# Performance work log

Hardware: AMD Instinct MI355X
Metric: run time of the kernel (lower is better)

Reference implementation:

```python
import jax, jax.numpy as jnp
import numpy as np

# Block-sparse layout constants (must match init_kwargs):
BS = 64       # block_size (= block_m = block_n)
NB = 64       # number of blocks per side -> max_seqlen = 4096
LOCAL = 8     # causal sliding window of 8 blocks
GLOBAL = 1    # 1 global (attention-sink) block


def _layout():
    """Build padded per-row block column indices and the token-level mask.

    Mirrors dkernel semantics: block (i, j) participates iff sparse_pattern[i, j] == 1,
    and within participating blocks a per-token causal mask (k_pos <= q_pos) is applied
    (dkernel applies causal masking on diagonal blocks; off-diagonal lower blocks pass
    the causal test trivially, so pattern & causal is exact).
    """
    i = np.arange(NB)[:, None]
    j = np.arange(NB)[None, :]
    pat = (j <= i) & (((i - j) < LOCAL) | (j < GLOBAL))  # [NB, NB] bool
    max_nnz = int(pat.sum(-1).max())                      # = LOCAL + GLOBAL = 9
    col = np.zeros((NB, max_nnz), np.int32)
    valid = np.zeros((NB, max_nnz), bool)
    for r in range(NB):
        idx = np.nonzero(pat[r])[0]
        col[r, :len(idx)] = idx
        valid[r, :len(idx)] = True
    # token positions
    qpos = np.arange(NB)[:, None] * BS + np.arange(BS)[None, :]                    # [NB, BS]
    kpos = (col[:, :, None] * BS + np.arange(BS)[None, None, :]).reshape(NB, -1)   # [NB, max_nnz*BS]
    vmask = np.repeat(valid, BS, axis=1)                                           # [NB, max_nnz*BS]
    mask = vmask[:, None, :] & (kpos[:, None, :] <= qpos[:, :, None])              # [NB, BS, max_nnz*BS]
    return col, mask

_COL, _MASK = _layout()


def setup_inputs() -> dict:
    key = jax.random.key(0)
    kq, kk, kv = jax.random.split(key, 3)
    B, S, H, D = 2, 4096, 16, 128
    q = jax.random.normal(kq, (B, S, H, D), dtype=jnp.float32)
    k = jax.random.normal(kk, (B, S, H, D), dtype=jnp.float32)
    v = jax.random.normal(kv, (B, S, H, D), dtype=jnp.float32)
    return {"q": q, "k": k, "v": v}


def reference(q, k, v):
    B, S, H, D = q.shape
    sm_scale = 1.0 / np.sqrt(float(D))  # default sm_scale in forward()
    # -> [B, H, NB, BS, D]
    qb = q.reshape(B, NB, BS, H, D).transpose(0, 3, 1, 2, 4)
    kb = k.reshape(B, NB, BS, H, D).transpose(0, 3, 1, 2, 4)
    vb = v.reshape(B, NB, BS, H, D).transpose(0, 3, 1, 2, 4)
    col = jnp.asarray(_COL)                              # [NB, max_nnz]
    # gather the kv blocks each q-block attends to: [B, H, NB, max_nnz*BS, D]
    kg = kb[:, :, col].reshape(B, H, NB, -1, D)
    vg = vb[:, :, col].reshape(B, H, NB, -1, D)
    # block-sparse scores: [B, H, NB, BS, max_nnz*BS]
    s = jnp.einsum('bhnqd,bhnkd->bhnqk', qb, kg) * sm_scale
    s = jnp.where(jnp.asarray(_MASK)[None, None], s, -jnp.inf)
    p = jax.nn.softmax(s, axis=-1)
    o = jnp.einsum('bhnqk,bhnkd->bhnqd', p, vg)          # [B, H, NB, BS, D]
    return o.transpose(0, 2, 3, 1, 4).reshape(B, S, H, D)
```

## Files before the change

kernel.cpp:

```cpp
#include <hip/hip_runtime.h>
#include <hip/hip_bf16.h>


typedef __bf16 bf16_t;
typedef bf16_t bf16x8 __attribute__((ext_vector_type(8)));
typedef float f32x4 __attribute__((ext_vector_type(4)));
typedef uint32_t u32x4 __attribute__((ext_vector_type(4)));

#define BSZ 64
#define DIM 128
#define NH 16
#define SEQ 4096
#define ROWSTRIDE (NH * DIM)

#define LGKM_BARRIER()                                          \
    do {                                                        \
        asm volatile("s_waitcnt lgkmcnt(0)" ::: "memory");      \
        __builtin_amdgcn_s_barrier();                           \
    } while (0)

__device__ __forceinline__ uint32_t cvt_pk_bf16(float lo, float hi) {
    uint32_t r;
    asm("v_cvt_pk_bf16_f32 %0, %1, %2" : "=v"(r) : "v"(lo), "v"(hi));
    return r;
}

__device__ __forceinline__ uint32_t kb_swz(uint32_t A) {
    return A ^ (((A >> 8) & 7u) << 4) ^ (((A >> 11) & 1u) << 7);
}
__device__ __forceinline__ uint32_t vt_swz(uint32_t A) {
    return A ^ (((A >> 9) & 7u) << 4) ^ (((A >> 9) & 1u) << 6) ^ (((A >> 12) & 3u) << 7);
}

__global__ __launch_bounds__(256) void sparse_attn_kernel(
    const float* __restrict__ q, const float* __restrict__ k,
    const float* __restrict__ v, float* __restrict__ out)
{
    __shared__ __align__(16) bf16_t Kb[BSZ * DIM];
    __shared__ __align__(16) bf16_t Vt[DIM * BSZ];

    const int L  = ((blockIdx.x & 7) << 8) | (blockIdx.x >> 3);
    const int qi = L & 63;
    const int h  = (L >> 6) & 15;
    const int b  = L >> 10;

    const int tid  = threadIdx.x;
    const int wave = tid >> 6;
    const int lane = tid & 63;
    const int lr = lane & 15;
    const int lk = lane >> 4;
    const int k0 = lk * 8;

    const int krr = tid >> 4;
    const int kc8 = tid & 15;
    const int vr  = tid >> 5;
    const int sc4 = tid & 31;

    const float scale2 = 0.12751649736230476f;

    const size_t bh_off = ((size_t)b * SEQ * NH + (size_t)h) * DIM;
    const float* kbh = k + bh_off;
    const float* vbh = v + bh_off;

    bf16x8 qf[4];
    {
        const float* qrow = q + bh_off + (size_t)(qi * 64 + wave * 16 + lr) * ROWSTRIDE;
        #pragma unroll
        for (int kk = 0; kk < 4; ++kk) {
            const float4 a0 = *(const float4*)(qrow + 32 * kk + k0);
            const float4 a1 = *(const float4*)(qrow + 32 * kk + k0 + 4);
            u32x4 w = {cvt_pk_bf16(a0.x * scale2, a0.y * scale2),
                       cvt_pk_bf16(a0.z * scale2, a0.w * scale2),
                       cvt_pk_bf16(a1.x * scale2, a1.y * scale2),
                       cvt_pk_bf16(a1.z * scale2, a1.w * scale2)};
            qf[kk] = *(bf16x8*)&w;
        }
    }

    f32x4 oacc[8];
    #pragma unroll
    for (int n = 0; n < 8; ++n) oacc[n] = (f32x4){0.f, 0.f, 0.f, 0.f};
    float lrun = 0.f;

    const int qrow_local = wave * 16 + lr;
    const int nnz = (qi < 8) ? (qi + 1) : 9;

    const int bit0 = lk & 1;
    const int bit1 = lk >> 1;
    const bool hi  = (lk & 2) != 0;
    const int Dlo  = (lr + 16 * bit1) << 2;
    const int Dhi  = Dlo + (32 << 2);
    const int addrA = bit0 ? Dhi : Dlo;
    const int addrB = bit0 ? Dlo : Dhi;

    float4 kreg[8];
    float4 vreg[8];

    #define LOAD_K(jb)                                                            \
    {                                                                             \
        _Pragma("unroll")                                                         \
        for (int i = 0; i < 4; ++i) {                                             \
            const float* p_ = kbh + (size_t)((jb) * 64 + 16 * i + krr) * ROWSTRIDE\
                              + 8 * kc8;                                          \
            kreg[2 * i]     = *(const float4*)(p_);                               \
            kreg[2 * i + 1] = *(const float4*)(p_ + 4);                           \
        }                                                                         \
    }
    #define LOAD_V(jb)                                                            \
    {                                                                             \
        const float* vb_ = vbh + (size_t)((jb) * 64 + 8 * vr) * ROWSTRIDE + 4 * sc4;\
        _Pragma("unroll")                                                         \
        for (int i = 0; i < 8; ++i)                                               \
            vreg[i] = *(const float4*)(vb_ + (size_t)i * ROWSTRIDE);              \
    }

    LOAD_K(0);
    LOAD_V(0);

    for (int t = 0; t < nnz; ++t) {
        const int j = (qi < 8) ? t : ((t == 0) ? 0 : (qi - 8 + t));
        const int jn = (qi < 8) ? (t + 1) : (qi - 8 + t + 1);
        const bool have_next = (t + 1 < nnz);

        #pragma unroll
        for (int i = 0; i < 4; ++i) {
            const float4 a0 = kreg[2 * i];
            const float4 a1 = kreg[2 * i + 1];
            u32x4 w = {cvt_pk_bf16(a0.x, a0.y), cvt_pk_bf16(a0.z, a0.w),
                       cvt_pk_bf16(a1.x, a1.y), cvt_pk_bf16(a1.z, a1.w)};
            const uint32_t A = kb_swz((uint32_t)((16 * i + krr) * 256 + 16 * kc8));
            *(u32x4*)((char*)Kb + A) = w;
        }
        if (have_next) { LOAD_K(jn); }

        LGKM_BARRIER();

        f32x4 sacc[4];
        #pragma unroll
        for (int n = 0; n < 4; ++n) {
            f32x4 a = (f32x4){0.f, 0.f, 0.f, 0.f};
            #pragma unroll
            for (int kk = 0; kk < 4; ++kk) {
                const uint32_t A = kb_swz((uint32_t)((16 * n + lr) * 256 + 64 * kk + 16 * lk));
                bf16x8 kf = *(const bf16x8*)((const char*)Kb + A);
                a = __builtin_amdgcn_mfma_f32_16x16x32_bf16(kf, qf[kk], a, 0, 0, 0);
            }
            sacc[n] = a;
        }

        #pragma unroll
        for (int j2 = 0; j2 < 4; ++j2) {
            u32x4 w = {cvt_pk_bf16(((const float*)&vreg[0])[j2], ((const float*)&vreg[1])[j2]),
                       cvt_pk_bf16(((const float*)&vreg[2])[j2], ((const float*)&vreg[3])[j2]),
                       cvt_pk_bf16(((const float*)&vreg[4])[j2], ((const float*)&vreg[5])[j2]),
                       cvt_pk_bf16(((const float*)&vreg[6])[j2], ((const float*)&vreg[7])[j2])};
            const int d = 4 * sc4 + j2;
            const uint32_t A = vt_swz((uint32_t)(d * 128 + 16 * vr));
            *(u32x4*)((char*)Vt + A) = w;
        }
        if (have_next) { LOAD_V(jn); }

        if (j == qi) {
            #pragma unroll
            for (int n = 0; n < 4; ++n)
                #pragma unroll
                for (int r = 0; r < 4; ++r) {
                    if (16 * n + 4 * lk + r > qrow_local) sacc[n][r] = -1.0e30f;
                }
        }

        uint32_t ch[8];
        #pragma unroll
        for (int n = 0; n < 4; ++n) {
            float p0 = exp2f(sacc[n][0]);
            float p1 = exp2f(sacc[n][1]);
            float p2 = exp2f(sacc[n][2]);
            float p3 = exp2f(sacc[n][3]);
            lrun += (p0 + p1) + (p2 + p3);
            ch[2 * n]     = cvt_pk_bf16(p0, p1);
            ch[2 * n + 1] = cvt_pk_bf16(p2, p3);
        }

        bf16x8 paf[2];
        #pragma unroll
        for (int kk = 0; kk < 2; ++kk) {
            uint32_t r0 = (uint32_t)__builtin_amdgcn_ds_permute(
                addrA, (int)(bit0 ? ch[4 * kk + 2] : ch[4 * kk + 0]));
            uint32_t r1 = (uint32_t)__builtin_amdgcn_ds_permute(
                addrA, (int)(bit0 ? ch[4 * kk + 3] : ch[4 * kk + 1]));
            uint32_t r2 = (uint32_t)__builtin_amdgcn_ds_permute(
                addrB, (int)(bit0 ? ch[4 * kk + 0] : ch[4 * kk + 2]));
            uint32_t r3 = (uint32_t)__builtin_amdgcn_ds_permute(
                addrB, (int)(bit0 ? ch[4 * kk + 1] : ch[4 * kk + 3]));
            u32x4 tv = {hi ? r2 : r0, hi ? r3 : r1,
                        hi ? r0 : r2, hi ? r1 : r3};
            paf[kk] = *(bf16x8*)&tv;
        }

        LGKM_BARRIER();

        #pragma unroll
        for (int n = 0; n < 8; ++n) {
            f32x4 a = oacc[n];
            #pragma unroll
            for (int kk = 0; kk < 2; ++kk) {
                const uint32_t Av = vt_swz((uint32_t)((16 * n + lr) * 128 + 64 * kk + 16 * lk));
                bf16x8 vf = *(const bf16x8*)((const char*)Vt + Av);
                a = __builtin_amdgcn_mfma_f32_16x16x32_bf16(paf[kk], vf, a, 0, 0, 0);
            }
            oacc[n] = a;
        }
    }

    float lrtot = lrun;
    lrtot += __shfl_xor(lrtot, 16);
    lrtot += __shfl_xor(lrtot, 32);
    float* obase = out + bh_off + (size_t)(qi * 64 + wave * 16) * ROWSTRIDE;
    #pragma unroll
    for (int r = 0; r < 4; ++r) {
        const float inv = 1.0f / __shfl(lrtot, 4 * lk + r);
        float* orow = obase + (size_t)(4 * lk + r) * ROWSTRIDE;
        #pragma unroll
        for (int n = 0; n < 8; ++n) {
            orow[16 * n + lr] = oacc[n][r] * inv;
        }
    }
}

extern "C" void kernel_launch(void* const* d_in, const int* in_sizes, int n_in,
                              void* d_out, int out_size, void* d_ws, size_t ws_size,
                              hipStream_t stream) {
    const float* q = (const float*)d_in[0];
    const float* k = (const float*)d_in[1];
    const float* v = (const float*)d_in[2];
    float* out = (float*)d_out;
    sparse_attn_kernel<<<dim3(2048), dim3(256), 0, stream>>>(q, k, v, out);
}
```

Before: 92.53 us.

## Add dedicated producer wave group with double-buffered K/V shared memory

Splits the block into four consumer waves that do the MFMA work and two producer waves that load K/V from global memory, convert them to bf16 and write them into double-buffered shared memory. Consumers no longer hold prefetch registers or do conversions, and producers and consumers hand off each block through one barrier per iteration. The aim is to overlap global loads and conversion with compute while cutting consumer register pressure. In exchange, shared memory per block doubles to 64KB and the block grows to 384 threads, which may lower occupancy, and the producers load serially in large batches.

```diff
diff --git a/kernel.cpp b/kernel.cpp
--- a/kernel.cpp
+++ b/kernel.cpp
@@ -32,35 +32,100 @@
     return A ^ (((A >> 9) & 7u) << 4) ^ (((A >> 9) & 1u) << 6) ^ (((A >> 12) & 3u) << 7);
 }
 
-__global__ __launch_bounds__(256) void sparse_attn_kernel(
+__global__ __launch_bounds__(384) void sparse_attn_kernel(
     const float* __restrict__ q, const float* __restrict__ k,
     const float* __restrict__ v, float* __restrict__ out)
 {
-    __shared__ __align__(16) bf16_t Kb[BSZ * DIM];
-    __shared__ __align__(16) bf16_t Vt[DIM * BSZ];
+    __shared__ __align__(16) bf16_t Kb[2 * BSZ * DIM];
+    __shared__ __align__(16) bf16_t Vt[2 * DIM * BSZ];
 
     const int L  = ((blockIdx.x & 7) << 8) | (blockIdx.x >> 3);
     const int qi = L & 63;
     const int h  = (L >> 6) & 15;
     const int b  = L >> 10;
 
-    const int tid  = threadIdx.x;
+    const int tid = threadIdx.x;
+
+    const size_t bh_off = ((size_t)b * SEQ * NH + (size_t)h) * DIM;
+    const float* kbh = k + bh_off;
+    const float* vbh = v + bh_off;
+    const int nnz = (qi < 8) ? (qi + 1) : 9;
+
+    if (tid >= 256) {
+        const int pl   = tid - 256;
+        const int krow = pl >> 4;
+        const int kch8 = pl & 15;
+        const int vrb  = pl >> 5;
+        const int sc4p = pl & 31;
+
+        #define PROD_STAGE(jb, bufOff)                                            \
+        {                                                                         \
+            const float* kb_ = kbh + (size_t)(jb) * 64 * ROWSTRIDE;               \
+            const float* vb_ = vbh + (size_t)(jb) * 64 * ROWSTRIDE;               \
+            float4 st[16];                                                        \
+            _Pragma("unroll")                                                     \
+            for (int i = 0; i < 8; ++i) {                                         \
+                const float* p_ = kb_ + (size_t)(krow + 8 * i) * ROWSTRIDE        \
+                                  + 8 * kch8;                                     \
+                st[2 * i]     = *(const float4*)p_;                               \
+                st[2 * i + 1] = *(const float4*)(p_ + 4);                         \
+            }                                                                     \
+            _Pragma("unroll")                                                     \
+            for (int i = 0; i < 8; ++i) {                                         \
+                const float4 a0 = st[2 * i], a1 = st[2 * i + 1];                  \
+                u32x4 w = {cvt_pk_bf16(a0.x, a0.y), cvt_pk_bf16(a0.z, a0.w),      \
+                           cvt_pk_bf16(a1.x, a1.y), cvt_pk_bf16(a1.z, a1.w)};     \
+                const uint32_t A = kb_swz((uint32_t)((krow + 8 * i) * 256         \
+                                                     + 16 * kch8));               \
+                *(u32x4*)((char*)Kb + (bufOff) + A) = w;                          \
+            }                                                                     \
+            _Pragma("unroll")                                                     \
+            for (int g = 0; g < 2; ++g) {                                         \
+                const int vrg = vrb + 4 * g;                                      \
+                const float* q_ = vb_ + (size_t)(8 * vrg) * ROWSTRIDE + 4 * sc4p; \
+                _Pragma("unroll")                                                 \
+                for (int i = 0; i < 8; ++i)                                       \
+                    st[8 * g + i] = *(const float4*)(q_ + (size_t)i * ROWSTRIDE); \
+            }                                                                     \
+            _Pragma("unroll")                                                     \
+            for (int g = 0; g < 2; ++g) {                                         \
+                const int vrg = vrb + 4 * g;                                      \
+                _Pragma("unroll")                                                 \
+                for (int j2 = 0; j2 < 4; ++j2) {                                  \
+                    u32x4 w = {cvt_pk_bf16(((const float*)&st[8*g+0])[j2],        \
+                                           ((const float*)&st[8*g+1])[j2]),       \
+                               cvt_pk_bf16(((const float*)&st[8*g+2])[j2],        \
+                                           ((const float*)&st[8*g+3])[j2]),       \
+                               cvt_pk_bf16(((const float*)&st[8*g+4])[j2],        \
+                                           ((const float*)&st[8*g+5])[j2]),       \
+                               cvt_pk_bf16(((const float*)&st[8*g+6])[j2],        \
+                                           ((const float*)&st[8*g+7])[j2])};      \
+                    const int d = 4 * sc4p + j2;                                  \
+                    const uint32_t A = vt_swz((uint32_t)(d * 128 + 16 * vrg));    \
+                    *(u32x4*)((char*)Vt + (bufOff) + A) = w;                      \
+                }                                                                 \
+            }                                                                     \
+        }
+
+        PROD_STAGE(0, 0);
+        LGKM_BARRIER();
+        for (int t = 0; t < nnz; ++t) {
+            if (t + 1 < nnz) {
+                const int jn = (qi < 8) ? (t + 1) : (qi - 8 + t + 1);
+                PROD_STAGE(jn, (uint32_t)(((t + 1) & 1) * 16384));
+            }
+            LGKM_BARRIER();
+        }
+        return;
+    }
+
     const int wave = tid >> 6;
     const int lane = tid & 63;
     const int lr = lane & 15;
     const int lk = lane >> 4;
     const int k0 = lk * 8;
 
-    const int krr = tid >> 4;
-    const int kc8 = tid & 15;
-    const int vr  = tid >> 5;
-    const int sc4 = tid & 31;
-
     const float scale2 = 0.12751649736230476f;
-
-    const size_t bh_off = ((size_t)b * SEQ * NH + (size_t)h) * DIM;
-    const float* kbh = k + bh_off;
-    const float* vbh = v + bh_off;
 
     bf16x8 qf[4];
     {
@@ -83,7 +148,6 @@
     float lrun = 0.f;
 
     const int qrow_local = wave * 16 + lr;
-    const int nnz = (qi < 8) ? (qi + 1) : 9;
 
     const int bit0 = lk & 1;
     const int bit1 = lk >> 1;
@@ -93,47 +157,11 @@
     const int addrA = bit0 ? Dhi : Dlo;
     const int addrB = bit0 ? Dlo : Dhi;
 
-    float4 kreg[8];
-    float4 vreg[8];
-
-    #define LOAD_K(jb)                                                            \
-    {                                                                             \
-        _Pragma("unroll")                                                         \
-        for (int i = 0; i < 4; ++i) {                                             \
-            const float* p_ = kbh + (size_t)((jb) * 64 + 16 * i + krr) * ROWSTRIDE\
-                              + 8 * kc8;                                          \
-            kreg[2 * i]     = *(const float4*)(p_);                               \
-            kreg[2 * i + 1] = *(const float4*)(p_ + 4);                           \
-        }                                                                         \
-    }
-    #define LOAD_V(jb)                                                            \
-    {                                                                             \
-        const float* vb_ = vbh + (size_t)((jb) * 64 + 8 * vr) * ROWSTRIDE + 4 * sc4;\
-        _Pragma("unroll")                                                         \
-        for (int i = 0; i < 8; ++i)                                               \
-            vreg[i] = *(const float4*)(vb_ + (size_t)i * ROWSTRIDE);              \
-    }
-
-    LOAD_K(0);
-    LOAD_V(0);
+    LGKM_BARRIER();
 
     for (int t = 0; t < nnz; ++t) {
         const int j = (qi < 8) ? t : ((t == 0) ? 0 : (qi - 8 + t));
-        const int jn = (qi < 8) ? (t + 1) : (qi - 8 + t + 1);
-        const bool have_next = (t + 1 < nnz);
-
-        #pragma unroll
-        for (int i = 0; i < 4; ++i) {
-            const float4 a0 = kreg[2 * i];
-            const float4 a1 = kreg[2 * i + 1];
-            u32x4 w = {cvt_pk_bf16(a0.x, a0.y), cvt_pk_bf16(a0.z, a0.w),
-                       cvt_pk_bf16(a1.x, a1.y), cvt_pk_bf16(a1.z, a1.w)};
-            const uint32_t A = kb_swz((uint32_t)((16 * i + krr) * 256 + 16 * kc8));
-            *(u32x4*)((char*)Kb + A) = w;
-        }
-        if (have_next) { LOAD_K(jn); }
-
-        LGKM_BARRIER();
+        const uint32_t bufOff = (uint32_t)((t & 1) * 16384);
 
         f32x4 sacc[4];
         #pragma unroll
@@ -142,23 +170,11 @@
             #pragma unroll
             for (int kk = 0; kk < 4; ++kk) {
                 const uint32_t A = kb_swz((uint32_t)((16 * n + lr) * 256 + 64 * kk + 16 * lk));
-                bf16x8 kf = *(const bf16x8*)((const char*)Kb + A);
+                bf16x8 kf = *(const bf16x8*)((const char*)Kb + bufOff + A);
                 a = __builtin_amdgcn_mfma_f32_16x16x32_bf16(kf, qf[kk], a, 0, 0, 0);
             }
             sacc[n] = a;
         }
-
-        #pragma unroll
-        for (int j2 = 0; j2 < 4; ++j2) {
-            u32x4 w = {cvt_pk_bf16(((const float*)&vreg[0])[j2], ((const float*)&vreg[1])[j2]),
-                       cvt_pk_bf16(((const float*)&vreg[2])[j2], ((const float*)&vreg[3])[j2]),
-                       cvt_pk_bf16(((const float*)&vreg[4])[j2], ((const float*)&vreg[5])[j2]),
-                       cvt_pk_bf16(((const float*)&vreg[6])[j2], ((const float*)&vreg[7])[j2])};
-            const int d = 4 * sc4 + j2;
-            const uint32_t A = vt_swz((uint32_t)(d * 128 + 16 * vr));
-            *(u32x4*)((char*)Vt + A) = w;
-        }
-        if (have_next) { LOAD_V(jn); }
 
         if (j == qi) {
             #pragma unroll
@@ -197,19 +213,19 @@
             paf[kk] = *(bf16x8*)&tv;
         }
 
-        LGKM_BARRIER();
-
         #pragma unroll
         for (int n = 0; n < 8; ++n) {
             f32x4 a = oacc[n];
             #pragma unroll
             for (int kk = 0; kk < 2; ++kk) {
                 const uint32_t Av = vt_swz((uint32_t)((16 * n + lr) * 128 + 64 * kk + 16 * lk));
-                bf16x8 vf = *(const bf16x8*)((const char*)Vt + Av);
+                bf16x8 vf = *(const bf16x8*)((const char*)Vt + bufOff + Av);
                 a = __builtin_amdgcn_mfma_f32_16x16x32_bf16(paf[kk], vf, a, 0, 0, 0);
             }
             oacc[n] = a;
         }
+
+        LGKM_BARRIER();
     }
 
     float lrtot = lrun;
@@ -234,5 +250,5 @@
     const float* k = (const float*)d_in[1];
     const float* v = (const float*)d_in[2];
     float* out = (float*)d_out;
-    sparse_attn_kernel<<<dim3(2048), dim3(256), 0, stream>>>(q, k, v, out);
-}
+    sparse_attn_kernel<<<dim3(2048), dim3(384), 0, stream>>>(q, k, v, out);
+}
```

Result: slower. 106.6 us (+15.2%).

## Double-buffer K/V tiles in LDS to drop one barrier per KV block

Applied to the files above, without the earlier changes.

Each K and V tile now goes into one of two LDS buffers that alternate, so the kernel writes both K and V for a tile together and needs a single barrier per tile instead of two. The loop is unrolled by two so the buffer offsets are compile-time constants, and the next tile's global loads are issued right after the current tile's LDS writes. This is meant to cut synchronisation stalls between waves. In exchange, LDS use per block doubles to 64 KB, which can lower how many blocks fit on a CU. V's global load latency is also hidden less, because V is written to LDS before the score computation rather than after it.

```diff
diff --git a/kernel.cpp b/kernel.cpp
--- a/kernel.cpp
+++ b/kernel.cpp
@@ -36,8 +36,8 @@
     const float* __restrict__ q, const float* __restrict__ k,
     const float* __restrict__ v, float* __restrict__ out)
 {
-    __shared__ __align__(16) bf16_t Kb[BSZ * DIM];
-    __shared__ __align__(16) bf16_t Vt[DIM * BSZ];
+    __shared__ __align__(16) bf16_t Kb[2 * BSZ * DIM];
+    __shared__ __align__(16) bf16_t Vt[2 * DIM * BSZ];
 
     const int L  = ((blockIdx.x & 7) << 8) | (blockIdx.x >> 3);
     const int qi = L & 63;
@@ -96,32 +96,24 @@
     float4 kreg[8];
     float4 vreg[8];
 
-    #define LOAD_K(jb)                                                            \
-    {                                                                             \
-        _Pragma("unroll")                                                         \
-        for (int i = 0; i < 4; ++i) {                                             \
-            const float* p_ = kbh + (size_t)((jb) * 64 + 16 * i + krr) * ROWSTRIDE\
-                              + 8 * kc8;                                          \
-            kreg[2 * i]     = *(const float4*)(p_);                               \
-            kreg[2 * i + 1] = *(const float4*)(p_ + 4);                           \
-        }                                                                         \
-    }
-    #define LOAD_V(jb)                                                            \
-    {                                                                             \
-        const float* vb_ = vbh + (size_t)((jb) * 64 + 8 * vr) * ROWSTRIDE + 4 * sc4;\
-        _Pragma("unroll")                                                         \
-        for (int i = 0; i < 8; ++i)                                               \
-            vreg[i] = *(const float4*)(vb_ + (size_t)i * ROWSTRIDE);              \
-    }
-
-    LOAD_K(0);
-    LOAD_V(0);
-
-    for (int t = 0; t < nnz; ++t) {
-        const int j = (qi < 8) ? t : ((t == 0) ? 0 : (qi - 8 + t));
-        const int jn = (qi < 8) ? (t + 1) : (qi - 8 + t + 1);
-        const bool have_next = (t + 1 < nnz);
-
+    auto j_of = [&](int t) -> int {
+        return (qi < 8) ? t : ((t == 0) ? 0 : (qi - 8 + t));
+    };
+
+    auto load_kv = [&](int jb) {
+        #pragma unroll
+        for (int i = 0; i < 4; ++i) {
+            const float* p_ = kbh + (size_t)(jb * 64 + 16 * i + krr) * ROWSTRIDE + 8 * kc8;
+            kreg[2 * i]     = *(const float4*)(p_);
+            kreg[2 * i + 1] = *(const float4*)(p_ + 4);
+        }
+        const float* vb_ = vbh + (size_t)(jb * 64 + 8 * vr) * ROWSTRIDE + 4 * sc4;
+        #pragma unroll
+        for (int i = 0; i < 8; ++i)
+            vreg[i] = *(const float4*)(vb_ + (size_t)i * ROWSTRIDE);
+    };
+
+    auto stage_write = [&](uint32_t off) {
         #pragma unroll
         for (int i = 0; i < 4; ++i) {
             const float4 a0 = kreg[2 * i];
@@ -129,25 +121,8 @@
             u32x4 w = {cvt_pk_bf16(a0.x, a0.y), cvt_pk_bf16(a0.z, a0.w),
                        cvt_pk_bf16(a1.x, a1.y), cvt_pk_bf16(a1.z, a1.w)};
             const uint32_t A = kb_swz((uint32_t)((16 * i + krr) * 256 + 16 * kc8));
-            *(u32x4*)((char*)Kb + A) = w;
-        }
-        if (have_next) { LOAD_K(jn); }
-
-        LGKM_BARRIER();
-
-        f32x4 sacc[4];
-        #pragma unroll
-        for (int n = 0; n < 4; ++n) {
-            f32x4 a = (f32x4){0.f, 0.f, 0.f, 0.f};
-            #pragma unroll
-            for (int kk = 0; kk < 4; ++kk) {
-                const uint32_t A = kb_swz((uint32_t)((16 * n + lr) * 256 + 64 * kk + 16 * lk));
-                bf16x8 kf = *(const bf16x8*)((const char*)Kb + A);
-                a = __builtin_amdgcn_mfma_f32_16x16x32_bf16(kf, qf[kk], a, 0, 0, 0);
-            }
-            sacc[n] = a;
-        }
-
+            *(u32x4*)((char*)Kb + off + A) = w;
+        }
         #pragma unroll
         for (int j2 = 0; j2 < 4; ++j2) {
             u32x4 w = {cvt_pk_bf16(((const float*)&vreg[0])[j2], ((const float*)&vreg[1])[j2]),
@@ -156,11 +131,24 @@
                        cvt_pk_bf16(((const float*)&vreg[6])[j2], ((const float*)&vreg[7])[j2])};
             const int d = 4 * sc4 + j2;
             const uint32_t A = vt_swz((uint32_t)(d * 128 + 16 * vr));
-            *(u32x4*)((char*)Vt + A) = w;
-        }
-        if (have_next) { LOAD_V(jn); }
-
-        if (j == qi) {
+            *(u32x4*)((char*)Vt + off + A) = w;
+        }
+    };
+
+    auto compute_tile = [&](int jj, uint32_t off) {
+        f32x4 sacc[4];
+        #pragma unroll
+        for (int n = 0; n < 4; ++n) {
+            f32x4 a = (f32x4){0.f, 0.f, 0.f, 0.f};
+            #pragma unroll
+            for (int kk = 0; kk < 4; ++kk) {
+                const uint32_t A = kb_swz((uint32_t)((16 * n + lr) * 256 + 64 * kk + 16 * lk));
+                bf16x8 kf = *(const bf16x8*)((const char*)Kb + off + A);
+                a = __builtin_amdgcn_mfma_f32_16x16x32_bf16(kf, qf[kk], a, 0, 0, 0);
+            }
+            sacc[n] = a;
+        }
+        if (jj == qi) {
             #pragma unroll
             for (int n = 0; n < 4; ++n)
                 #pragma unroll
@@ -168,7 +156,6 @@
                     if (16 * n + 4 * lk + r > qrow_local) sacc[n][r] = -1.0e30f;
                 }
         }
-
         uint32_t ch[8];
         #pragma unroll
         for (int n = 0; n < 4; ++n) {
@@ -180,7 +167,6 @@
             ch[2 * n]     = cvt_pk_bf16(p0, p1);
             ch[2 * n + 1] = cvt_pk_bf16(p2, p3);
         }
-
         bf16x8 paf[2];
         #pragma unroll
         for (int kk = 0; kk < 2; ++kk) {
@@ -196,19 +182,31 @@
                         hi ? r0 : r2, hi ? r1 : r3};
             paf[kk] = *(bf16x8*)&tv;
         }
-
-        LGKM_BARRIER();
-
         #pragma unroll
         for (int n = 0; n < 8; ++n) {
             f32x4 a = oacc[n];
             #pragma unroll
             for (int kk = 0; kk < 2; ++kk) {
                 const uint32_t Av = vt_swz((uint32_t)((16 * n + lr) * 128 + 64 * kk + 16 * lk));
-                bf16x8 vf = *(const bf16x8*)((const char*)Vt + Av);
+                bf16x8 vf = *(const bf16x8*)((const char*)Vt + off + Av);
                 a = __builtin_amdgcn_mfma_f32_16x16x32_bf16(paf[kk], vf, a, 0, 0, 0);
             }
             oacc[n] = a;
+        }
+    };
+
+    load_kv(0);
+
+    for (int t = 0; t < nnz; t += 2) {
+        stage_write(0);
+        if (t + 1 < nnz) { load_kv(j_of(t + 1)); }
+        LGKM_BARRIER();
+        compute_tile(j_of(t), 0);
+        if (t + 1 < nnz) {
+            stage_write(16384);
+            if (t + 2 < nnz) { load_kv(j_of(t + 2)); }
+            LGKM_BARRIER();
+            compute_tile(j_of(t + 1), 16384);
         }
     }
 
```

Result: slower. 96.05 us (+3.8%).
